# Optimization experiments

Hardware: AMD Instinct MI355X
Metric: run time of the kernel (lower is better)

Reference implementation:

```python
import jax, jax.numpy as jnp
import numpy as np

B, S, D = 4, 1024, 2048
H, G = 16, 2            # num_heads, num_groups (GQA)
HD = D // H             # head_dim = 128


def rotate_half(x):
    x1, x2 = x[..., : x.shape[-1] // 2], x[..., x.shape[-1] // 2 :]
    return jnp.concatenate([-x2, x1], axis=-1)


def setup_inputs() -> dict:
    key = jax.random.key(0)
    ks = jax.random.split(key, 9)
    scale = 0.02
    return {
        "x": jax.random.normal(ks[0], (B, S, D), jnp.float32),
        "wq": jax.random.normal(ks[1], (D, D), jnp.float32) * scale,
        "bq": jnp.zeros((D,), jnp.float32),
        "wk": jax.random.normal(ks[2], (D, G * HD), jnp.float32) * scale,
        "bk": jnp.zeros((G * HD,), jnp.float32),
        "wv": jax.random.normal(ks[3], (D, G * HD), jnp.float32) * scale,
        "bv": jnp.zeros((G * HD,), jnp.float32),
        "wo": jax.random.normal(ks[4], (D, D), jnp.float32) * scale,
        "bo": jnp.zeros((D,), jnp.float32),
    }


def reference(x, wq, bq, wk, bk, wv, bv, wo, bo):
    b, s, d = x.shape
    hd = HD
    # projections (flax Linear: y = x @ kernel + bias)
    q = (x @ wq + bq).reshape(b, s, H, hd)
    k = (x @ wk + bk).reshape(b, s, G, hd)
    v = (x @ wv + bv).reshape(b, s, G, hd)

    # RoPE tables (positions = arange(s), matching q_pos/kv_pos defaults)
    inv_freq = 1.0 / 10000 ** (jnp.arange(0, hd, 2, dtype=jnp.float32) / hd)
    t = jnp.arange(s, dtype=jnp.float32)
    freqs = jnp.outer(t, inv_freq)              # [s, hd/2]
    freqs = jnp.concatenate([freqs, freqs], -1)  # [s, hd]
    sin = jnp.sin(freqs)[:, None, :]             # [s, 1, hd]
    cos = jnp.cos(freqs)[:, None, :]

    q = q * cos + rotate_half(q) * sin
    q = q * (hd ** -0.5)  # module's explicit scale
    k = k * cos + rotate_half(k) * sin

    # GQA: expand K/V groups to full heads (repeats = H // G)
    reps = H // G
    k_exp = jnp.repeat(k, reps, axis=2)  # [b, s, H, hd]
    v_exp = jnp.repeat(v, reps, axis=2)

    # jax.nn.dot_product_attention also applies 1/sqrt(hd) by default,
    # so net scaling is hd**-1 (faithful to the original module).
    scores = jnp.einsum("bqhd,bkhd->bhqk", q, k_exp) * (hd ** -0.5)
    attn = jax.nn.softmax(scores, axis=-1)
    out = jnp.einsum("bhqk,bkhd->bqhd", attn, v_exp).reshape(b, s, d)
    return out @ wo + bo
```

## Files before the change

kernel.cpp:

```cpp
#include <hip/hip_runtime.h>
#include <hip/hip_bf16.h>
#include <type_traits>

typedef __attribute__((ext_vector_type(8))) __bf16 bf16x8;
typedef __attribute__((ext_vector_type(4))) float floatx4;

__device__ inline floatx4 mfma_bf16(bf16x8 a, bf16x8 b, floatx4 c) {
    return __builtin_amdgcn_mfma_f32_16x16x32_bf16(a, b, c, 0, 0, 0);
}

__device__ inline void g2l16(const __hip_bfloat16* g, __hip_bfloat16* l) {
    __builtin_amdgcn_global_load_lds(
        (const __attribute__((address_space(1))) void*)g,
        (__attribute__((address_space(3))) void*)l, 16, 0, 0);
}

__global__ void cast_f32_bf16_k(const float* __restrict__ in,
                                __hip_bfloat16* __restrict__ out, int n4) {
    int i = blockIdx.x * blockDim.x + threadIdx.x;
    if (i < n4) {
        float4 v = ((const float4*)in)[i];
        ushort4 u;
        __hip_bfloat16 a0 = __float2bfloat16(v.x), a1 = __float2bfloat16(v.y);
        __hip_bfloat16 a2 = __float2bfloat16(v.z), a3 = __float2bfloat16(v.w);
        u.x = *(unsigned short*)&a0; u.y = *(unsigned short*)&a1;
        u.z = *(unsigned short*)&a2; u.w = *(unsigned short*)&a3;
        ((ushort4*)out)[i] = u;
    }
}

__global__ void prep_k(const float* __restrict__ wq, const float* __restrict__ wk,
                       const float* __restrict__ wv, const float* __restrict__ wo,
                       const float* __restrict__ bq, const float* __restrict__ bk,
                       const float* __restrict__ bv,
                       __hip_bfloat16* __restrict__ wqkvt,
                       __hip_bfloat16* __restrict__ wot,
                       float* __restrict__ bqkv) {
    int bid = blockIdx.x;
    if (bid >= 9216) {
        int i = (bid - 9216) * 256 + threadIdx.x;
        if (i < 2560)
            bqkv[i] = (i < 2048) ? bq[i] : (i < 2304 ? bk[i - 2048] : bv[i - 2304]);
        return;
    }
    const float* W; __hip_bfloat16* Wt; int C, row_off, cb, rb;
    if (bid < 4096)      { W = wq; Wt = wqkvt; C = 2048; row_off = 0;
                           cb = bid & 63; rb = bid >> 6; }
    else if (bid < 4608) { W = wk; Wt = wqkvt; C = 256;  row_off = 2048;
                           int id = bid - 4096; cb = id & 7; rb = id >> 3; }
    else if (bid < 5120) { W = wv; Wt = wqkvt; C = 256;  row_off = 2304;
                           int id = bid - 4608; cb = id & 7; rb = id >> 3; }
    else                 { W = wo; Wt = wot;   C = 2048; row_off = 0;
                           int id = bid - 5120; cb = id & 63; rb = id >> 6; }
    __shared__ float tile[32][33];
    int c0 = cb * 32, r0 = rb * 32;
    int tx = threadIdx.x & 31, ty0 = threadIdx.x >> 5;
#pragma unroll
    for (int i = 0; i < 4; i++) {
        int ty = ty0 + i * 8;
        tile[ty][tx] = W[(size_t)(r0 + ty) * C + c0 + tx];
    }
    __syncthreads();
#pragma unroll
    for (int i = 0; i < 4; i++) {
        int ty = ty0 + i * 8;
        Wt[(size_t)(row_off + c0 + ty) * 2048 + r0 + tx] = __float2bfloat16(tile[tx][ty]);
    }
}

__global__ __launch_bounds__(256) void gemm_qkv_k(
    const __hip_bfloat16* __restrict__ A,
    const __hip_bfloat16* __restrict__ Bt,
    const float* __restrict__ bias,
    __hip_bfloat16* __restrict__ Qb,
    __hip_bfloat16* __restrict__ Kb,
    __hip_bfloat16* __restrict__ Vlin) {
    __shared__ alignas(16) __hip_bfloat16 As[128 * 32];
    __shared__ alignas(16) __hip_bfloat16 Bs[128 * 32];
    const int t = threadIdx.x, lane = t & 63, w = t >> 6;
    const int quad = lane >> 4, l16 = lane & 15;
    const int bm = blockIdx.y, bn = blockIdx.x;
    const int r_ = t >> 2;
    const int kc_ = (t & 3) ^ ((t >> 3) & 3);
    const int swz = (l16 >> 1) & 3;

    const __hip_bfloat16* gA = A + (size_t)(bm * 128 + r_) * 2048 + kc_ * 8;
    const __hip_bfloat16* gB = Bt + (size_t)(bn * 128 + r_) * 2048 + kc_ * 8;

    floatx4 acc[2][8] = {};

    for (int kt = 0; kt < 2048; kt += 32) {
        g2l16(gA + kt, As + t * 8);
        g2l16(gA + kt + 64 * 2048, As + (t + 256) * 8);
        g2l16(gB + kt, Bs + t * 8);
        g2l16(gB + kt + 64 * 2048, Bs + (t + 256) * 8);
        __syncthreads();
        bf16x8 af[2], bfr[8];
#pragma unroll
        for (int mi = 0; mi < 2; mi++)
            af[mi] = *(const bf16x8*)(As + (w * 32 + mi * 16 + l16) * 32 + (quad ^ swz) * 8);
#pragma unroll
        for (int ni = 0; ni < 8; ni++)
            bfr[ni] = *(const bf16x8*)(Bs + (ni * 16 + l16) * 32 + (quad ^ swz) * 8);
#pragma unroll
        for (int mi = 0; mi < 2; mi++)
#pragma unroll
            for (int ni = 0; ni < 8; ni++)
                acc[mi][ni] = mfma_bf16(af[mi], bfr[ni], acc[mi][ni]);
        __syncthreads();
    }

    const int row_base = bm * 128 + w * 32 + quad * 4;
    if (bn < 18) {
        const float scale = (bn < 16) ? 0.0078125f : 1.0f;
        __hip_bfloat16* dst = (bn < 16) ? Qb : Kb;
        const int nh = (bn < 16) ? 16 : 2;
        const int hh = (bn < 16) ? bn : (bn - 16);
#pragma unroll
        for (int ni = 0; ni < 4; ni++) {
            int j = ni * 16 + l16;
            float invf = __expf(-(float)j * (9.210340371976184f / 64.f));
            float bj  = bias[bn * 128 + j];
            float bj2 = bias[bn * 128 + j + 64];
#pragma unroll
            for (int mi = 0; mi < 2; mi++)
#pragma unroll
                for (int r = 0; r < 4; r++) {
                    int row = row_base + mi * 16 + r;
                    int b = row >> 10, s = row & 1023;
                    float vj  = acc[mi][ni][r] + bj;
                    float vj2 = acc[mi][ni + 4][r] + bj2;
                    float sn, cs;
                    __sincosf((float)s * invf, &sn, &cs);
                    __hip_bfloat16* op = dst + ((size_t)(b * nh + hh) * 1024 + s) * 128;
                    op[j]      = __float2bfloat16((vj * cs - vj2 * sn) * scale);
                    op[j + 64] = __float2bfloat16((vj2 * cs + vj * sn) * scale);
                }
        }
    } else {
        int g = bn - 18;
#pragma unroll
        for (int ni = 0; ni < 8; ni++) {
            int col = ni * 16 + l16;
            float bv = bias[bn * 128 + col];
#pragma unroll
            for (int mi = 0; mi < 2; mi++)
#pragma unroll
                for (int r = 0; r < 4; r++) {
                    int row = row_base + mi * 16 + r;
                    Vlin[(size_t)row * 256 + g * 128 + col] =
                        __float2bfloat16(acc[mi][ni][r] + bv);
                }
        }
    }
}

template <typename OUT_T>
__global__ __launch_bounds__(256) void gemm_bt_k(
    const __hip_bfloat16* __restrict__ A,
    const __hip_bfloat16* __restrict__ Bt,
    const float* __restrict__ bias,
    OUT_T* __restrict__ C,
    int M, int N, int K) {
    __shared__ alignas(16) __hip_bfloat16 As[128 * 32];
    __shared__ alignas(16) __hip_bfloat16 Bs[128 * 32];
    const int t = threadIdx.x;
    const int lane = t & 63;
    const int w = t >> 6;
    const int wm = w & 1, wn = w >> 1;
    const int quad = lane >> 4, l16 = lane & 15;
    const int bm = blockIdx.y, bn = blockIdx.x;
    const int r_ = t >> 2;
    const int kc_ = (t & 3) ^ ((t >> 3) & 3);
    const int swz = (l16 >> 1) & 3;

    const __hip_bfloat16* gA = A + (size_t)(bm * 128 + r_) * K + kc_ * 8;
    const __hip_bfloat16* gB = Bt + (size_t)(bn * 128 + r_) * K + kc_ * 8;

    floatx4 acc[4][4] = {};

    for (int kt = 0; kt < K; kt += 32) {
        g2l16(gA + kt, As + t * 8);
        g2l16(gA + kt + (size_t)64 * K, As + (t + 256) * 8);
        g2l16(gB + kt, Bs + t * 8);
        g2l16(gB + kt + (size_t)64 * K, Bs + (t + 256) * 8);
        __syncthreads();
        bf16x8 af[4], bfr[4];
#pragma unroll
        for (int mi = 0; mi < 4; mi++)
            af[mi] = *(const bf16x8*)(As + (wm * 64 + mi * 16 + l16) * 32 + (quad ^ swz) * 8);
#pragma unroll
        for (int ni = 0; ni < 4; ni++)
            bfr[ni] = *(const bf16x8*)(Bs + (wn * 64 + ni * 16 + l16) * 32 + (quad ^ swz) * 8);
#pragma unroll
        for (int mi = 0; mi < 4; mi++)
#pragma unroll
            for (int ni = 0; ni < 4; ni++)
                acc[mi][ni] = mfma_bf16(af[mi], bfr[ni], acc[mi][ni]);
        __syncthreads();
    }

#pragma unroll
    for (int mi = 0; mi < 4; mi++) {
        int row0 = bm * 128 + wm * 64 + mi * 16 + quad * 4;
#pragma unroll
        for (int ni = 0; ni < 4; ni++) {
            int col = bn * 128 + wn * 64 + ni * 16 + l16;
            float bv = bias[col];
#pragma unroll
            for (int r = 0; r < 4; r++) {
                float v = acc[mi][ni][r] + bv;
                if constexpr (std::is_same<OUT_T, float>::value)
                    C[(size_t)(row0 + r) * N + col] = v;
                else
                    C[(size_t)(row0 + r) * N + col] = __float2bfloat16(v);
            }
        }
    }
}

__global__ void transpose_v_k(const __hip_bfloat16* __restrict__ Vlin,
                              __hip_bfloat16* __restrict__ VT) {
    __shared__ __hip_bfloat16 tile[32][33];
    int bg = blockIdx.z;
    int b = bg >> 1, g = bg & 1;
    int s0 = blockIdx.y * 32, d0 = blockIdx.x * 32;
    int tx = threadIdx.x & 31, ty0 = threadIdx.x >> 5;
#pragma unroll
    for (int i = 0; i < 4; i++) {
        int ty = ty0 + i * 8;
        tile[ty][tx] = Vlin[(size_t)(b * 1024 + s0 + ty) * 256 + g * 128 + d0 + tx];
    }
    __syncthreads();
#pragma unroll
    for (int i = 0; i < 4; i++) {
        int ty = ty0 + i * 8;
        VT[((size_t)(b * 2 + g) * 128 + d0 + ty) * 1024 + s0 + tx] = tile[tx][ty];
    }
}

__global__ __launch_bounds__(256, 2) void attn_k(
    const __hip_bfloat16* __restrict__ Qb,
    const __hip_bfloat16* __restrict__ Kb,
    const __hip_bfloat16* __restrict__ VT,
    __hip_bfloat16* __restrict__ AO) {
    constexpr int PLD = 72;
    __shared__ alignas(16) __hip_bfloat16 Ks[64 * 128];
    __shared__ alignas(16) __hip_bfloat16 Vs[128 * 64];
    __shared__ alignas(16) __hip_bfloat16 Ps[4][32 * PLD];

    const int bh = blockIdx.x;
    const int b = bh >> 4, h = bh & 15, g = h >> 3;
    const int t = threadIdx.x, lane = t & 63, w = t >> 6;
    const int quad = lane >> 4, l16 = lane & 15;
    const int q0 = blockIdx.y * 128 + w * 32;

    const __hip_bfloat16* Qp = Qb + ((size_t)bh * 1024 + q0 + l16) * 128 + quad * 8;
    bf16x8 aq[2][4];
#pragma unroll
    for (int mi = 0; mi < 2; mi++)
#pragma unroll
        for (int kc = 0; kc < 4; kc++)
            aq[mi][kc] = *(const bf16x8*)(Qp + mi * 16 * 128 + kc * 32);

    const int bg = b * 2 + g;
    const __hip_bfloat16* Kstage = Kb + (size_t)bg * 1024 * 128
        + (t >> 4) * 128 + ((t & 15) ^ (t >> 4)) * 8;
    const __hip_bfloat16* Vstage = VT + (size_t)bg * 128 * 1024
        + (t >> 3) * 1024 + ((t & 7) ^ ((t >> 3) & 7)) * 8;

    float l_part[2][4] = {};
    floatx4 o[2][8] = {};

    for (int kv = 0; kv < 1024; kv += 64) {
#pragma unroll
        for (int j = 0; j < 4; j++)
            g2l16(Kstage + (size_t)(kv + j * 16) * 128, Ks + (j * 256 + t) * 8);
#pragma unroll
        for (int j = 0; j < 4; j++)
            g2l16(Vstage + (size_t)j * 32 * 1024 + kv, Vs + (j * 256 + t) * 8);
        __syncthreads();

        floatx4 s[2][4] = {};
#pragma unroll
        for (int nj = 0; nj < 4; nj++)
#pragma unroll
            for (int kc = 0; kc < 4; kc++) {
                bf16x8 kb = *(const bf16x8*)(Ks + (nj * 16 + l16) * 128
                                             + (((kc * 4 + quad) ^ l16) * 8));
                s[0][nj] = mfma_bf16(aq[0][kc], kb, s[0][nj]);
                s[1][nj] = mfma_bf16(aq[1][kc], kb, s[1][nj]);
            }

        __hip_bfloat16* pl = Ps[w];
#pragma unroll
        for (int mi = 0; mi < 2; mi++)
#pragma unroll
            for (int nj = 0; nj < 4; nj++)
#pragma unroll
                for (int r = 0; r < 4; r++) {
                    float p = __expf(s[mi][nj][r]);
                    l_part[mi][r] += p;
                    pl[(mi * 16 + quad * 4 + r) * PLD + nj * 16 + l16] =
                        __float2bfloat16(p);
                }
        asm volatile("s_waitcnt lgkmcnt(0)" ::: "memory");

        bf16x8 ap[2][2];
#pragma unroll
        for (int mi = 0; mi < 2; mi++)
#pragma unroll
            for (int kc2 = 0; kc2 < 2; kc2++)
                ap[mi][kc2] = *(const bf16x8*)(pl + (mi * 16 + l16) * PLD
                                               + kc2 * 32 + quad * 8);

#pragma unroll
        for (int ni = 0; ni < 8; ni++)
#pragma unroll
            for (int kc2 = 0; kc2 < 2; kc2++) {
                bf16x8 vb = *(const bf16x8*)(Vs + (ni * 16 + l16) * 64
                                             + (((kc2 * 4 + quad) ^ (l16 & 7)) * 8));
                o[0][ni] = mfma_bf16(ap[0][kc2], vb, o[0][ni]);
                o[1][ni] = mfma_bf16(ap[1][kc2], vb, o[1][ni]);
            }
        __syncthreads();
    }

#pragma unroll
    for (int mi = 0; mi < 2; mi++)
#pragma unroll
        for (int r = 0; r < 4; r++) {
            float sum = l_part[mi][r];
            sum += __shfl_xor(sum, 1);
            sum += __shfl_xor(sum, 2);
            sum += __shfl_xor(sum, 4);
            sum += __shfl_xor(sum, 8);
            float inv = 1.f / sum;
            size_t srow = (size_t)b * 1024 + q0 + mi * 16 + quad * 4 + r;
#pragma unroll
            for (int ni = 0; ni < 8; ni++)
                AO[srow * 2048 + h * 128 + ni * 16 + l16] =
                    __float2bfloat16(o[mi][ni][r] * inv);
        }
}

extern "C" void kernel_launch(void* const* d_in, const int* in_sizes, int n_in,
                              void* d_out, int out_size, void* d_ws, size_t ws_size,
                              hipStream_t stream) {
    (void)in_sizes; (void)n_in; (void)out_size; (void)ws_size;
    const float* x  = (const float*)d_in[0];
    const float* wq = (const float*)d_in[1];
    const float* bq = (const float*)d_in[2];
    const float* wk = (const float*)d_in[3];
    const float* bk = (const float*)d_in[4];
    const float* wv = (const float*)d_in[5];
    const float* bv = (const float*)d_in[6];
    const float* wo = (const float*)d_in[7];
    const float* bo = (const float*)d_in[8];
    float* out = (float*)d_out;

    char* ws = (char*)d_ws;
    __hip_bfloat16* xb    = (__hip_bfloat16*)(ws + 0);
    __hip_bfloat16* AO    = xb;
    __hip_bfloat16* wqkvt = (__hip_bfloat16*)(ws + 16777216);
    __hip_bfloat16* wot   = (__hip_bfloat16*)(ws + 27262976);
    __hip_bfloat16* Qb    = (__hip_bfloat16*)(ws + 35651584);
    __hip_bfloat16* Kb    = (__hip_bfloat16*)(ws + 52428800);
    __hip_bfloat16* Vlin  = (__hip_bfloat16*)(ws + 54525952);
    __hip_bfloat16* VT    = (__hip_bfloat16*)(ws + 56623104);
    float*          bqkv  = (float*)(ws + 58720256);

    cast_f32_bf16_k<<<8192, 256, 0, stream>>>(x, xb, 2097152);
    prep_k<<<9226, 256, 0, stream>>>(wq, wk, wv, wo, bq, bk, bv, wqkvt, wot, bqkv);
    gemm_qkv_k<<<dim3(20, 32), 256, 0, stream>>>(xb, wqkvt, bqkv, Qb, Kb, Vlin);
    transpose_v_k<<<dim3(4, 32, 8), 256, 0, stream>>>(Vlin, VT);
    attn_k<<<dim3(64, 8), 256, 0, stream>>>(Qb, Kb, VT, AO);
    gemm_bt_k<float><<<dim3(16, 32), 256, 0, stream>>>(AO, wot, bo, out, 4096, 2048, 2048);
}
```

Before: 280.1 us.

## Halve per-wave query rows in attention and merge prep kernels into one launch

The attention kernel now gives each wave 16 query rows instead of 32, which doubles the grid to 64x16 blocks and raises the launch-bounds occupancy hint from 2 to 3. The aim is more parallelism and latency hiding through lower register and LDS use. The cost is that each K/V tile staged in LDS now feeds half as many query rows, so the same K/V data gets loaded twice as often. Separately, the x cast and the weight/bias prep kernels are merged into one launch to save a kernel launch.

```diff
diff --git a/kernel.cpp b/kernel.cpp
--- a/kernel.cpp
+++ b/kernel.cpp
@@ -15,28 +15,28 @@
         (__attribute__((address_space(3))) void*)l, 16, 0, 0);
 }
 
-__global__ void cast_f32_bf16_k(const float* __restrict__ in,
-                                __hip_bfloat16* __restrict__ out, int n4) {
-    int i = blockIdx.x * blockDim.x + threadIdx.x;
-    if (i < n4) {
-        float4 v = ((const float4*)in)[i];
+__global__ void prep_all_k(const float* __restrict__ x,
+                           __hip_bfloat16* __restrict__ xb,
+                           const float* __restrict__ wq, const float* __restrict__ wk,
+                           const float* __restrict__ wv, const float* __restrict__ wo,
+                           const float* __restrict__ bq, const float* __restrict__ bk,
+                           const float* __restrict__ bv,
+                           __hip_bfloat16* __restrict__ wqkvt,
+                           __hip_bfloat16* __restrict__ wot,
+                           float* __restrict__ bqkv) {
+    int bid0 = blockIdx.x;
+    if (bid0 < 8192) {
+        int i = bid0 * 256 + threadIdx.x;
+        float4 v = ((const float4*)x)[i];
         ushort4 u;
         __hip_bfloat16 a0 = __float2bfloat16(v.x), a1 = __float2bfloat16(v.y);
         __hip_bfloat16 a2 = __float2bfloat16(v.z), a3 = __float2bfloat16(v.w);
         u.x = *(unsigned short*)&a0; u.y = *(unsigned short*)&a1;
         u.z = *(unsigned short*)&a2; u.w = *(unsigned short*)&a3;
-        ((ushort4*)out)[i] = u;
-    }
-}
-
-__global__ void prep_k(const float* __restrict__ wq, const float* __restrict__ wk,
-                       const float* __restrict__ wv, const float* __restrict__ wo,
-                       const float* __restrict__ bq, const float* __restrict__ bk,
-                       const float* __restrict__ bv,
-                       __hip_bfloat16* __restrict__ wqkvt,
-                       __hip_bfloat16* __restrict__ wot,
-                       float* __restrict__ bqkv) {
-    int bid = blockIdx.x;
+        ((ushort4*)xb)[i] = u;
+        return;
+    }
+    int bid = bid0 - 8192;
     if (bid >= 9216) {
         int i = (bid - 9216) * 256 + threadIdx.x;
         if (i < 2560)
@@ -239,7 +239,7 @@
     }
 }
 
-__global__ __launch_bounds__(256, 2) void attn_k(
+__global__ __launch_bounds__(256, 3) void attn_k(
     const __hip_bfloat16* __restrict__ Qb,
     const __hip_bfloat16* __restrict__ Kb,
     const __hip_bfloat16* __restrict__ VT,
@@ -247,21 +247,19 @@
     constexpr int PLD = 72;
     __shared__ alignas(16) __hip_bfloat16 Ks[64 * 128];
     __shared__ alignas(16) __hip_bfloat16 Vs[128 * 64];
-    __shared__ alignas(16) __hip_bfloat16 Ps[4][32 * PLD];
+    __shared__ alignas(16) __hip_bfloat16 Ps[4][16 * PLD];
 
     const int bh = blockIdx.x;
     const int b = bh >> 4, h = bh & 15, g = h >> 3;
     const int t = threadIdx.x, lane = t & 63, w = t >> 6;
     const int quad = lane >> 4, l16 = lane & 15;
-    const int q0 = blockIdx.y * 128 + w * 32;
+    const int q0 = blockIdx.y * 64 + w * 16;
 
     const __hip_bfloat16* Qp = Qb + ((size_t)bh * 1024 + q0 + l16) * 128 + quad * 8;
-    bf16x8 aq[2][4];
-#pragma unroll
-    for (int mi = 0; mi < 2; mi++)
-#pragma unroll
-        for (int kc = 0; kc < 4; kc++)
-            aq[mi][kc] = *(const bf16x8*)(Qp + mi * 16 * 128 + kc * 32);
+    bf16x8 aq[4];
+#pragma unroll
+    for (int kc = 0; kc < 4; kc++)
+        aq[kc] = *(const bf16x8*)(Qp + kc * 32);
 
     const int bg = b * 2 + g;
     const __hip_bfloat16* Kstage = Kb + (size_t)bg * 1024 * 128
@@ -269,8 +267,8 @@
     const __hip_bfloat16* Vstage = VT + (size_t)bg * 128 * 1024
         + (t >> 3) * 1024 + ((t & 7) ^ ((t >> 3) & 7)) * 8;
 
-    float l_part[2][4] = {};
-    floatx4 o[2][8] = {};
+    float l_part[4] = {};
+    floatx4 o[8] = {};
 
     for (int kv = 0; kv < 1024; kv += 64) {
 #pragma unroll
@@ -281,38 +279,31 @@
             g2l16(Vstage + (size_t)j * 32 * 1024 + kv, Vs + (j * 256 + t) * 8);
         __syncthreads();
 
-        floatx4 s[2][4] = {};
+        floatx4 s[4] = {};
 #pragma unroll
         for (int nj = 0; nj < 4; nj++)
 #pragma unroll
             for (int kc = 0; kc < 4; kc++) {
                 bf16x8 kb = *(const bf16x8*)(Ks + (nj * 16 + l16) * 128
                                              + (((kc * 4 + quad) ^ l16) * 8));
-                s[0][nj] = mfma_bf16(aq[0][kc], kb, s[0][nj]);
-                s[1][nj] = mfma_bf16(aq[1][kc], kb, s[1][nj]);
+                s[nj] = mfma_bf16(aq[kc], kb, s[nj]);
             }
 
         __hip_bfloat16* pl = Ps[w];
 #pragma unroll
-        for (int mi = 0; mi < 2; mi++)
-#pragma unroll
-            for (int nj = 0; nj < 4; nj++)
-#pragma unroll
-                for (int r = 0; r < 4; r++) {
-                    float p = __expf(s[mi][nj][r]);
-                    l_part[mi][r] += p;
-                    pl[(mi * 16 + quad * 4 + r) * PLD + nj * 16 + l16] =
-                        __float2bfloat16(p);
-                }
+        for (int nj = 0; nj < 4; nj++)
+#pragma unroll
+            for (int r = 0; r < 4; r++) {
+                float p = __expf(s[nj][r]);
+                l_part[r] += p;
+                pl[(quad * 4 + r) * PLD + nj * 16 + l16] = __float2bfloat16(p);
+            }
         asm volatile("s_waitcnt lgkmcnt(0)" ::: "memory");
 
-        bf16x8 ap[2][2];
-#pragma unroll
-        for (int mi = 0; mi < 2; mi++)
-#pragma unroll
-            for (int kc2 = 0; kc2 < 2; kc2++)
-                ap[mi][kc2] = *(const bf16x8*)(pl + (mi * 16 + l16) * PLD
-                                               + kc2 * 32 + quad * 8);
+        bf16x8 ap[2];
+#pragma unroll
+        for (int kc2 = 0; kc2 < 2; kc2++)
+            ap[kc2] = *(const bf16x8*)(pl + l16 * PLD + kc2 * 32 + quad * 8);
 
 #pragma unroll
         for (int ni = 0; ni < 8; ni++)
@@ -320,28 +311,25 @@
             for (int kc2 = 0; kc2 < 2; kc2++) {
                 bf16x8 vb = *(const bf16x8*)(Vs + (ni * 16 + l16) * 64
                                              + (((kc2 * 4 + quad) ^ (l16 & 7)) * 8));
-                o[0][ni] = mfma_bf16(ap[0][kc2], vb, o[0][ni]);
-                o[1][ni] = mfma_bf16(ap[1][kc2], vb, o[1][ni]);
+                o[ni] = mfma_bf16(ap[kc2], vb, o[ni]);
             }
         __syncthreads();
     }
 
 #pragma unroll
-    for (int mi = 0; mi < 2; mi++)
-#pragma unroll
-        for (int r = 0; r < 4; r++) {
-            float sum = l_part[mi][r];
-            sum += __shfl_xor(sum, 1);
-            sum += __shfl_xor(sum, 2);
-            sum += __shfl_xor(sum, 4);
-            sum += __shfl_xor(sum, 8);
-            float inv = 1.f / sum;
-            size_t srow = (size_t)b * 1024 + q0 + mi * 16 + quad * 4 + r;
-#pragma unroll
-            for (int ni = 0; ni < 8; ni++)
-                AO[srow * 2048 + h * 128 + ni * 16 + l16] =
-                    __float2bfloat16(o[mi][ni][r] * inv);
-        }
+    for (int r = 0; r < 4; r++) {
+        float sum = l_part[r];
+        sum += __shfl_xor(sum, 1);
+        sum += __shfl_xor(sum, 2);
+        sum += __shfl_xor(sum, 4);
+        sum += __shfl_xor(sum, 8);
+        float inv = 1.f / sum;
+        size_t srow = (size_t)b * 1024 + q0 + quad * 4 + r;
+#pragma unroll
+        for (int ni = 0; ni < 8; ni++)
+            AO[srow * 2048 + h * 128 + ni * 16 + l16] =
+                __float2bfloat16(o[ni][r] * inv);
+    }
 }
 
 extern "C" void kernel_launch(void* const* d_in, const int* in_sizes, int n_in,
@@ -370,10 +358,10 @@
     __hip_bfloat16* VT    = (__hip_bfloat16*)(ws + 56623104);
     float*          bqkv  = (float*)(ws + 58720256);
 
-    cast_f32_bf16_k<<<8192, 256, 0, stream>>>(x, xb, 2097152);
-    prep_k<<<9226, 256, 0, stream>>>(wq, wk, wv, wo, bq, bk, bv, wqkvt, wot, bqkv);
+    prep_all_k<<<17418, 256, 0, stream>>>(x, xb, wq, wk, wv, wo, bq, bk, bv,
+                                          wqkvt, wot, bqkv);
     gemm_qkv_k<<<dim3(20, 32), 256, 0, stream>>>(xb, wqkvt, bqkv, Qb, Kb, Vlin);
     transpose_v_k<<<dim3(4, 32, 8), 256, 0, stream>>>(Vlin, VT);
-    attn_k<<<dim3(64, 8), 256, 0, stream>>>(Qb, Kb, VT, AO);
+    attn_k<<<dim3(64, 16), 256, 0, stream>>>(Qb, Kb, VT, AO);
     gemm_bt_k<float><<<dim3(16, 32), 256, 0, stream>>>(AO, wot, bo, out, 4096, 2048, 2048);
 }
```

New measurement: 287.3 us. 1.03x slower.
